# Kernel tuning notes

Measured on AMD Instinct MI355X. Metric: run time of the kernel, lower is better.

Reference implementation:

```python
import jax, jax.numpy as jnp
import numpy as np


def setup_inputs() -> dict:
    key = jax.random.key(0)
    k1, k2, k3, k4 = jax.random.split(key, 4)
    N, E, D_IN, D_OUT = 8192, 262144, 128, 128
    x = jax.random.normal(k1, (N, D_IN), dtype=jnp.float32)
    edge_index = jax.random.randint(k2, (2, E), 0, N, dtype=jnp.int64)
    # nn.Linear(in, out): weight [out, in], bias [out]
    W = jax.random.normal(k3, (D_OUT, D_IN), dtype=jnp.float32) / np.sqrt(D_IN)
    b = jax.random.normal(k4, (D_OUT,), dtype=jnp.float32) * 0.01
    return {"x": x, "edge_index": edge_index, "W": W, "b": b}


def reference(x, edge_index, W, b):
    N = x.shape[0]
    # Dense adjacency via scatter-set (duplicates collapse to 1.0), then add I.
    adj = jnp.zeros((N, N), dtype=x.dtype)
    adj = adj.at[edge_index[0], edge_index[1]].set(1.0)
    adj = adj + jnp.eye(N, dtype=x.dtype)
    # Symmetric normalization D^{-1/2} A D^{-1/2}; diag-matmul == row/col scaling.
    degree = adj.sum(axis=1)
    d_inv_sqrt = jnp.where(degree > 0, 1.0 / jnp.sqrt(degree), 0.0)
    adj_norm = adj * d_inv_sqrt[:, None] * d_inv_sqrt[None, :]
    # Aggregate then linear (eval mode: dropout inactive).
    out = adj_norm @ x              # [N, D_in]
    out = out @ W.T + b             # [N, D_out]
    return out
```

## Files before the change

kernel.cpp:

```cpp
#include <hip/hip_runtime.h>
#include <hip/hip_bf16.h>
#include <hip/hip_fp16.h>
#include <stdint.h>

#define N_NODES 8192
#define DIM 128
#define NBR_STRIDE 512
#define POISON32 0xAAAAAAAAu

__device__ __forceinline__ unsigned decode_cnt(unsigned v) {
    return v >= 0x80000000u ? v - POISON32 : v;
}

__global__ __launch_bounds__(256) void scatter_gemm(
        const void* __restrict__ eiv, int E,
        unsigned* __restrict__ cnt,
        int* __restrict__ nbr,
        const float* __restrict__ x,
        const float* __restrict__ W,
        __half* __restrict__ z) {
    const int t = threadIdx.x;
    const int b = blockIdx.x;

    if (b < 256) {
        const int* e32 = (const int*)eiv;
        const long long* e64 = (const long long*)eiv;
        bool is64 = (e32[1] == 0) && (e32[3] == 0) && (e32[5] == 0) &&
                    ((e32[0] | e32[2] | e32[4]) != 0);
        const int tid = b * 256 + t;
        for (int k = tid; k < E; k += 65536) {
            int r, c;
            if (is64) {
                r = (int)e64[k];
                c = (int)e64[E + k];
            } else {
                r = e32[k];
                c = e32[E + k];
            }
            if ((unsigned)r >= N_NODES || (unsigned)c >= N_NODES) continue;
            unsigned pos = decode_cnt(atomicAdd(&cnt[r], 1u));
            if (pos < NBR_STRIDE) nbr[r * NBR_STRIDE + pos] = c;
        }
        return;
    }

    __shared__ float xs[64 * 129];
    const int gb = b - 256;
    const int row_tile = gb >> 1;
    const int do_half = (gb & 1) * 64;
    const int row0 = row_tile * 64;

    const float4* xg = (const float4*)(x + (size_t)row0 * DIM);
    for (int i = t; i < 64 * 32; i += 256) {
        float4 v = xg[i];
        int r = i >> 5;
        int din = (i & 31) << 2;
        float* p = &xs[r * 129 + din];
        p[0] = v.x; p[1] = v.y; p[2] = v.z; p[3] = v.w;
    }
    __syncthreads();

    const int lane = t & 63;
    const int wave = __builtin_amdgcn_readfirstlane(t >> 6);
    const int row = row0 + lane;
    const float* xr = &xs[lane * 129];
    const int dob = do_half + wave * 8;

    float acc[16];
    #pragma unroll
    for (int j = 0; j < 16; ++j) acc[j] = 0.f;

    for (int din = 0; din < DIM; ++din) {
        float xv = xr[din];
        #pragma unroll
        for (int j = 0; j < 8; ++j) {
            acc[j]     += xv * W[(dob + j) * DIM + din];
            acc[8 + j] += xv * W[(dob + 32 + j) * DIM + din];
        }
    }
    __half* zp = z + (size_t)row * DIM;
    #pragma unroll
    for (int j = 0; j < 8; j += 2) {
        ((__half2*)(zp + dob))[j >> 1] =
            __floats2half2_rn(acc[j], acc[j + 1]);
        ((__half2*)(zp + dob + 32))[j >> 1] =
            __floats2half2_rn(acc[8 + j], acc[8 + j + 1]);
    }
}

__global__ __launch_bounds__(256) void dedup_deg(
        const unsigned* __restrict__ cnt,
        int* __restrict__ nbr,
        int* __restrict__ deg,
        float* __restrict__ dinv) {
    __shared__ int buf[4][NBR_STRIDE];
    const int lane = threadIdx.x & 63;
    const int w = threadIdx.x >> 6;
    const int row = blockIdx.x * 4 + w;

    int k = (int)decode_cnt(cnt[row]);
    if (k > NBR_STRIDE) k = NBR_STRIDE;
    int* lst = nbr + row * NBR_STRIDE;

    for (int i = lane; i < k; i += 64) buf[w][i] = lst[i];
    __syncthreads();

    int uniq = 0;
    for (int b0 = 0; b0 < k; b0 += 64) {
        const int idx = b0 + lane;
        const int c = (idx < k) ? buf[w][idx] : -1;
        bool dup = false;
        for (int j = 0; j < b0; ++j)
            dup |= (c == buf[w][j]);
        const int ilim = (k - b0 < 64 ? k - b0 : 64) - 1;
        for (int i = 0; i < ilim; ++i) {
            int vi = __shfl(c, i);
            dup |= (lane > i) & (c == vi);
        }
        const bool keep = (idx < k) && !dup;
        const unsigned long long m = __ballot(keep);
        const int rank = uniq + (int)__popcll(m & ((1ull << lane) - 1ull));
        if (keep) lst[rank] = c;
        uniq += (int)__popcll(m);
    }
    if (lane == 0) {
        deg[row] = uniq;
        dinv[row] = 1.0f / sqrtf((float)(uniq + 1));
    }
}

__global__ __launch_bounds__(256) void aggregate(
        const int* __restrict__ nbr,
        const int* __restrict__ deg,
        const float* __restrict__ dinv,
        const __half* __restrict__ z,
        const float* __restrict__ bias,
        float* __restrict__ out) {
    const int lane = threadIdx.x & 63;
    const int row = __builtin_amdgcn_readfirstlane(
        blockIdx.x * 4 + (threadIdx.x >> 6));
    const int lim = deg[row];
    const int* lst = nbr + row * NBR_STRIDE;

    float2 acc = {0.f, 0.f};
    int k = 0;
    for (; k + 8 <= lim; k += 8) {
        int4 j0 = *(const int4*)(lst + k);
        int4 j1 = *(const int4*)(lst + k + 4);
        __half2 h0 = ((const __half2*)(z + (size_t)j0.x * DIM))[lane];
        __half2 h1 = ((const __half2*)(z + (size_t)j0.y * DIM))[lane];
        __half2 h2 = ((const __half2*)(z + (size_t)j0.z * DIM))[lane];
        __half2 h3 = ((const __half2*)(z + (size_t)j0.w * DIM))[lane];
        __half2 h4 = ((const __half2*)(z + (size_t)j1.x * DIM))[lane];
        __half2 h5 = ((const __half2*)(z + (size_t)j1.y * DIM))[lane];
        __half2 h6 = ((const __half2*)(z + (size_t)j1.z * DIM))[lane];
        __half2 h7 = ((const __half2*)(z + (size_t)j1.w * DIM))[lane];
        float w0 = dinv[j0.x], w1 = dinv[j0.y];
        float w2 = dinv[j0.z], w3 = dinv[j0.w];
        float w4 = dinv[j1.x], w5 = dinv[j1.y];
        float w6 = dinv[j1.z], w7 = dinv[j1.w];
        float2 a0 = __half22float2(h0), a1 = __half22float2(h1);
        float2 a2 = __half22float2(h2), a3 = __half22float2(h3);
        float2 a4 = __half22float2(h4), a5 = __half22float2(h5);
        float2 a6 = __half22float2(h6), a7 = __half22float2(h7);
        acc.x += w0 * a0.x + w1 * a1.x + w2 * a2.x + w3 * a3.x
               + w4 * a4.x + w5 * a5.x + w6 * a6.x + w7 * a7.x;
        acc.y += w0 * a0.y + w1 * a1.y + w2 * a2.y + w3 * a3.y
               + w4 * a4.y + w5 * a5.y + w6 * a6.y + w7 * a7.y;
    }
    for (; k < lim; ++k) {
        int j = lst[k];
        float wj = dinv[j];
        float2 a = __half22float2(((const __half2*)(z + (size_t)j * DIM))[lane]);
        acc.x += wj * a.x;
        acc.y += wj * a.y;
    }

    float di = dinv[row];
    float2 zs = __half22float2(((const __half2*)(z + (size_t)row * DIM))[lane]);
    float2 bv = ((const float2*)bias)[lane];
    float2 res;
    res.x = di * acc.x + di * di * zs.x + bv.x;
    res.y = di * acc.y + di * di * zs.y + bv.y;
    ((float2*)(out + (size_t)row * DIM))[lane] = res;
}

extern "C" void kernel_launch(void* const* d_in, const int* in_sizes, int n_in,
                              void* d_out, int out_size, void* d_ws, size_t ws_size,
                              hipStream_t stream) {
    const float* x  = (const float*)d_in[0];
    const void*  ei = d_in[1];
    const float* W  = (const float*)d_in[2];
    const float* bb = (const float*)d_in[3];
    float* out = (float*)d_out;

    uint8_t* ws = (uint8_t*)d_ws;
    unsigned* cnt = (unsigned*)ws;
    int* deg      = (int*)(ws + 32u * 1024u);
    float* dinv   = (float*)(ws + 64u * 1024u);
    int* nbr      = (int*)(ws + 1024u * 1024u);
    __half* z     = (__half*)(ws + 17u * 1024u * 1024u);

    int E = in_sizes[1] / 2;

    scatter_gemm<<<512, 256, 0, stream>>>(ei, E, cnt, nbr, x, W, z);
    dedup_deg<<<N_NODES / 4, 256, 0, stream>>>(cnt, nbr, deg, dinv);
    aggregate<<<N_NODES / 4, 256, 0, stream>>>(nbr, deg, dinv, z, bb, out);
}
```

Before: 99.87 us.

## Pad neighbor lists with zero sentinel, drop aggregate tail loop, widen scatter grid

The scatter phase now uses 768 blocks instead of 256 to spread the edge atomics wider, and the grid grows so the GEMM blocks keep their count. Dedup no longer stages the list in LDS. It only compares against the already-unique prefix and pads each list to a multiple of 8 with a sentinel index N_NODES. That sentinel points to a zeroed extra z row and a zero dinv entry. The aggregate kernel then runs only the 8-wide unrolled loop with no scalar tail, at the cost of a few extra gathers of the sentinel row and dedup reads going straight to global or cache memory.

New measurement: 102.5 us. +2.7%, slower.

```diff
diff --git a/kernel.cpp b/kernel.cpp
--- a/kernel.cpp
+++ b/kernel.cpp
@@ -22,13 +22,13 @@
     const int t = threadIdx.x;
     const int b = blockIdx.x;
 
-    if (b < 256) {
+    if (b < 768) {
         const int* e32 = (const int*)eiv;
         const long long* e64 = (const long long*)eiv;
         bool is64 = (e32[1] == 0) && (e32[3] == 0) && (e32[5] == 0) &&
                     ((e32[0] | e32[2] | e32[4]) != 0);
         const int tid = b * 256 + t;
-        for (int k = tid; k < E; k += 65536) {
+        for (int k = tid; k < E; k += 196608) {
             int r, c;
             if (is64) {
                 r = (int)e64[k];
@@ -45,7 +45,10 @@
     }
 
     __shared__ float xs[64 * 129];
-    const int gb = b - 256;
+    const int gb = b - 768;
+    if (gb == 0 && t < 64) {
+        ((float*)(z + (size_t)N_NODES * DIM))[t] = 0.f;
+    }
     const int row_tile = gb >> 1;
     const int do_half = (gb & 1) * 64;
     const int row0 = row_tile * 64;
@@ -93,27 +96,24 @@
         int* __restrict__ nbr,
         int* __restrict__ deg,
         float* __restrict__ dinv) {
-    __shared__ int buf[4][NBR_STRIDE];
     const int lane = threadIdx.x & 63;
-    const int w = threadIdx.x >> 6;
-    const int row = blockIdx.x * 4 + w;
+    const int row = __builtin_amdgcn_readfirstlane(
+        blockIdx.x * 4 + (threadIdx.x >> 6));
+    if (blockIdx.x == 0 && threadIdx.x == 0) dinv[N_NODES] = 0.f;
 
     int k = (int)decode_cnt(cnt[row]);
     if (k > NBR_STRIDE) k = NBR_STRIDE;
     int* lst = nbr + row * NBR_STRIDE;
 
-    for (int i = lane; i < k; i += 64) buf[w][i] = lst[i];
-    __syncthreads();
-
     int uniq = 0;
     for (int b0 = 0; b0 < k; b0 += 64) {
         const int idx = b0 + lane;
-        const int c = (idx < k) ? buf[w][idx] : -1;
+        const int c = (idx < k) ? lst[idx] : -1;
         bool dup = false;
-        for (int j = 0; j < b0; ++j)
-            dup |= (c == buf[w][j]);
-        const int ilim = (k - b0 < 64 ? k - b0 : 64) - 1;
-        for (int i = 0; i < ilim; ++i) {
+        for (int j = 0; j < uniq; ++j)
+            dup |= (c == lst[j]);
+        const int nvalid = (k - b0 < 64) ? (k - b0) : 64;
+        for (int i = 0; i < nvalid - 1; ++i) {
             int vi = __shfl(c, i);
             dup |= (lane > i) & (c == vi);
         }
@@ -123,6 +123,8 @@
         if (keep) lst[rank] = c;
         uniq += (int)__popcll(m);
     }
+    const int padded = (uniq + 7) & ~7;
+    if (lane < padded - uniq) lst[uniq + lane] = N_NODES;
     if (lane == 0) {
         deg[row] = uniq;
         dinv[row] = 1.0f / sqrtf((float)(uniq + 1));
@@ -139,12 +141,11 @@
     const int lane = threadIdx.x & 63;
     const int row = __builtin_amdgcn_readfirstlane(
         blockIdx.x * 4 + (threadIdx.x >> 6));
-    const int lim = deg[row];
+    const int lim8 = (deg[row] + 7) & ~7;
     const int* lst = nbr + row * NBR_STRIDE;
 
     float2 acc = {0.f, 0.f};
-    int k = 0;
-    for (; k + 8 <= lim; k += 8) {
+    for (int k = 0; k < lim8; k += 8) {
         int4 j0 = *(const int4*)(lst + k);
         int4 j1 = *(const int4*)(lst + k + 4);
         __half2 h0 = ((const __half2*)(z + (size_t)j0.x * DIM))[lane];
@@ -168,13 +169,6 @@
         acc.y += w0 * a0.y + w1 * a1.y + w2 * a2.y + w3 * a3.y
                + w4 * a4.y + w5 * a5.y + w6 * a6.y + w7 * a7.y;
     }
-    for (; k < lim; ++k) {
-        int j = lst[k];
-        float wj = dinv[j];
-        float2 a = __half22float2(((const __half2*)(z + (size_t)j * DIM))[lane]);
-        acc.x += wj * a.x;
-        acc.y += wj * a.y;
-    }
 
     float di = dinv[row];
     float2 zs = __half22float2(((const __half2*)(z + (size_t)row * DIM))[lane]);
@@ -203,7 +197,7 @@
 
     int E = in_sizes[1] / 2;
 
-    scatter_gemm<<<512, 256, 0, stream>>>(ei, E, cnt, nbr, x, W, z);
+    scatter_gemm<<<1024, 256, 0, stream>>>(ei, E, cnt, nbr, x, W, z);
     dedup_deg<<<N_NODES / 4, 256, 0, stream>>>(cnt, nbr, deg, dinv);
     aggregate<<<N_NODES / 4, 256, 0, stream>>>(nbr, deg, dinv, z, bb, out);
 }
```
